# Performance work log

Hardware: AMD Instinct MI355X
Metric: run time of the kernel (lower is better)

The kernel has to match this reference:

```python
import jax, jax.numpy as jnp
import numpy as np

BS, C, H, W = 2, 128, 80, 160
P, G = 9, 8
GC = C // G
EPS = 1e-5


def _layernorm_c(x, g, b):
    # x: (bs, C, H, W); LayerNorm over channel dim (to_3d dim=2 -> norm over c)
    m = jnp.mean(x, axis=1, keepdims=True)
    v = jnp.mean((x - m) ** 2, axis=1, keepdims=True)
    return (x - m) / jnp.sqrt(v + EPS) * g[None, :, None, None] + b[None, :, None, None]


def _conv1x1(x, w, b):
    return jnp.einsum('bchw,oc->bohw', x, w) + b[None, :, None, None]


def _bilinear_sample(feat, pts):
    # feat (bs,C,H,W); pts (bs,N,2) normalized [0,1]; zero padding outside (DAF convention)
    bs, c, h, w = feat.shape
    x = pts[..., 0] * w - 0.5
    y = pts[..., 1] * h - 0.5
    x0 = jnp.floor(x)
    y0 = jnp.floor(y)
    dx = x - x0
    dy = y - y0
    x0i = x0.astype(jnp.int32)
    y0i = y0.astype(jnp.int32)

    def corner(xi, yi, wgt):
        valid = (xi >= 0) & (xi < w) & (yi >= 0) & (yi < h)
        xc = jnp.clip(xi, 0, w - 1)
        yc = jnp.clip(yi, 0, h - 1)
        g = jax.vmap(lambda f, yy, xx: f[:, yy, xx].T)(feat, yc, xc)  # (bs,N,C)
        return g * (wgt * valid)[..., None]

    return (corner(x0i, y0i, (1 - dx) * (1 - dy))
            + corner(x0i + 1, y0i, dx * (1 - dy))
            + corner(x0i, y0i + 1, (1 - dx) * dy)
            + corner(x0i + 1, y0i + 1, dx * dy))


def _branch(match_flat, anchor, feat_value, wmap, kp_w, kp_b):
    bs = feat_value.shape[0]
    hw = H * W
    # Sparse1DKeyPointsGenerator: learned 1D offsets along the disparity (x) direction
    off = match_flat @ kp_w.T + kp_b  # (bs, HW, P)
    anc = anchor.reshape(bs, hw, P, 2)
    kp = jnp.stack([anc[..., 0] + off, anc[..., 1]], axis=-1)  # (bs,HW,P,2)
    # group-softmax attention weights over num_pts
    wts = wmap.transpose(0, 2, 3, 1).reshape(bs, hw, P, G)  # channel c = p*G + g
    wts = jax.nn.softmax(wts, axis=2)
    # deformable aggregation: bilinear gather at key points + group-weighted sum over pts
    sampled = _bilinear_sample(feat_value, kp.reshape(bs, hw * P, 2))
    sampled = sampled.reshape(bs, hw, P, G, GC)
    out = jnp.einsum('bnpgc,bnpg->bngc', sampled, wts).reshape(bs, hw, C)
    out = out.reshape(bs, H, W, C).transpose(0, 3, 1, 2)
    return out, kp


def _forward(mask, match, context, geometric, context_anchor_points, geometric_anchor_points,
             ln_g, ln_b, lnc_g, lnc_b, lng_g, lng_b,
             wc_w, wc_b, wg_w, wg_b, vc_w, vc_b, vg_w, vg_b,
             out_w, out_b, kpc_w, kpc_b, kpg_w, kpg_b):
    bs = match.shape[0]
    hw = H * W
    match_n = _layernorm_c(match, ln_g, ln_b)
    context_n = _layernorm_c(context, lnc_g, lnc_b)
    geometric_n = _layernorm_c(geometric, lng_g, lng_b)
    ctx_val = _conv1x1(context_n, vc_w, vc_b)
    geo_val = _conv1x1(geometric_n, vg_w, vg_b)
    match_flat = match_n.reshape(bs, C, hw).transpose(0, 2, 1)  # (bs,HW,C)
    wc = _conv1x1(match_n, wc_w, wc_b)  # (bs,G*P,H,W)
    wg = _conv1x1(match_n, wg_w, wg_b)
    ctx_out, ctx_kp = _branch(match_flat, context_anchor_points, ctx_val, wc, kpc_w, kpc_b)
    geo_out, geo_kp = _branch(match_flat, geometric_anchor_points, geo_val, wg, kpg_w, kpg_b)
    out = jnp.concatenate([ctx_out * mask, geo_out], axis=1)
    out = _conv1x1(out, out_w, out_b)  # proj_drop is identity (p=0)
    return out, ctx_kp.reshape(bs, H, W, P, 2), geo_kp.reshape(bs, H, W, P, 2)


def setup_inputs() -> dict:
    key = jax.random.key(0)
    ks = jax.random.split(key, 20)

    def wn(k, shape):
        return jax.random.normal(k, shape, jnp.float32) * 0.02

    return {
        'mask': jax.random.uniform(ks[0], (BS, 1, H, W), jnp.float32),
        'match': jax.random.normal(ks[1], (BS, C, H, W), jnp.float32),
        'context': jax.random.normal(ks[2], (BS, C, H, W), jnp.float32),
        'geometric': jax.random.normal(ks[3], (BS, C, H, W), jnp.float32),
        'context_anchor_points': jax.random.uniform(ks[4], (BS, H, W, P, 2), jnp.float32),
        'geometric_anchor_points': jax.random.uniform(ks[5], (BS, H, W, P, 2), jnp.float32),
        'ln_g': jnp.ones((C,), jnp.float32), 'ln_b': jnp.zeros((C,), jnp.float32),
        'lnc_g': jnp.ones((C,), jnp.float32), 'lnc_b': jnp.zeros((C,), jnp.float32),
        'lng_g': jnp.ones((C,), jnp.float32), 'lng_b': jnp.zeros((C,), jnp.float32),
        'wc_w': wn(ks[6], (G * P, C)), 'wc_b': jnp.zeros((G * P,), jnp.float32),
        'wg_w': wn(ks[7], (G * P, C)), 'wg_b': jnp.zeros((G * P,), jnp.float32),
        'vc_w': wn(ks[8], (C, C)), 'vc_b': jnp.zeros((C,), jnp.float32),
        'vg_w': wn(ks[9], (C, C)), 'vg_b': jnp.zeros((C,), jnp.float32),
        'out_w': wn(ks[10], (C, 2 * C)), 'out_b': jnp.zeros((C,), jnp.float32),
        'kpc_w': wn(ks[11], (P, C)), 'kpc_b': jnp.zeros((P,), jnp.float32),
        'kpg_w': wn(ks[12], (P, C)), 'kpg_b': jnp.zeros((P,), jnp.float32),
    }


def reference(mask, match, context, geometric, context_anchor_points, geometric_anchor_points,
              ln_g, ln_b, lnc_g, lnc_b, lng_g, lng_b,
              wc_w, wc_b, wg_w, wg_b, vc_w, vc_b, vg_w, vg_b,
              out_w, out_b, kpc_w, kpc_b, kpg_w, kpg_b):
    return _forward(mask, match, context, geometric, context_anchor_points, geometric_anchor_points,
                    ln_g, ln_b, lnc_g, lnc_b, lng_g, lng_b,
                    wc_w, wc_b, wg_w, wg_b, vc_w, vc_b, vg_w, vg_b,
                    out_w, out_b, kpc_w, kpc_b, kpg_w, kpg_b)
```

## Files before the change

kernel.cpp:

```cpp
#include <hip/hip_runtime.h>
#include <hip/hip_bf16.h>

typedef __hip_bfloat16 bf16;
typedef __bf16 b16x8 __attribute__((ext_vector_type(8)));
typedef float f32x4 __attribute__((ext_vector_type(4)));

#define HWs   12800
#define NPIX  25600
#define IMG_H 80
#define IMG_W 160

#define OFF_VCB  0
#define OFF_VGB  16384
#define OFF_MATB 32768
#define OFF_OUTB 53504
#define NW_BF16  86272

__global__ __launch_bounds__(256) void k_prep(
    const float* __restrict__ vc_w, const float* __restrict__ vg_w,
    const float* __restrict__ wc_w, const float* __restrict__ wg_w,
    const float* __restrict__ kpc_w, const float* __restrict__ kpg_w,
    const float* __restrict__ out_w,
    const float* __restrict__ wc_b, const float* __restrict__ wg_b,
    const float* __restrict__ kpc_b, const float* __restrict__ kpg_b,
    bf16* __restrict__ wbuf, float* __restrict__ bias176)
{
    int i = blockIdx.x * 256 + threadIdx.x;
    if (i < 16384) {
        wbuf[i] = __float2bfloat16(vc_w[i]);
    } else if (i < 32768) {
        wbuf[i] = __float2bfloat16(vg_w[i - 16384]);
    } else if (i < 53504) {
        int j = i - 32768; int row = j >> 7; int c = j & 127;
        float v;
        if (row < 72)       v = wc_w[row * 128 + c];
        else if (row < 144) v = wg_w[(row - 72) * 128 + c];
        else if (row < 153) v = kpc_w[(row - 144) * 128 + c];
        else                v = kpg_w[(row - 153) * 128 + c];
        wbuf[i] = __float2bfloat16(v);
    } else if (i < NW_BF16) {
        wbuf[i] = __float2bfloat16(out_w[i - 53504]);
    } else if (i < NW_BF16 + 176) {
        int j = i - NW_BF16;
        float v = 0.f;
        if (j < 72)       v = wc_b[j];
        else if (j < 144) v = wg_b[j - 72];
        else if (j < 153) v = kpc_b[j - 144];
        else if (j < 162) v = kpg_b[j - 153];
        bias176[j] = v;
    }
}

__global__ __launch_bounds__(256) void k_stage1(
    const float* __restrict__ match, const float* __restrict__ context, const float* __restrict__ geometric,
    const float* __restrict__ ln_g, const float* __restrict__ ln_b,
    const float* __restrict__ lnc_g, const float* __restrict__ lnc_b,
    const float* __restrict__ lng_g, const float* __restrict__ lng_b,
    const float* __restrict__ vc_b, const float* __restrict__ vg_b,
    const bf16* __restrict__ wbuf, const float* __restrict__ bias176,
    const float* __restrict__ anc_c, const float* __restrict__ anc_g,
    bf16* __restrict__ ctx_val, bf16* __restrict__ geo_val,
    bf16* __restrict__ wts_g, float* __restrict__ coords_g,
    float* __restrict__ kp_out)
{
    __shared__ __align__(16) bf16 tile_s[32 * 136];
    __shared__ bf16 logit_s[32 * 144];
    __shared__ float offs_s[32 * 18];
    __shared__ float red1[8][32];
    __shared__ float red2[8][32];

    int bx = blockIdx.x;
    int seg = bx / 800;
    int tile = bx - seg * 800;
    int t = threadIdx.x;
    int pixbase = tile * 32;

    const float* X  = (seg == 0) ? context : (seg == 1) ? geometric : match;
    const float* gg = (seg == 0) ? lnc_g   : (seg == 1) ? lng_g     : ln_g;
    const float* bb = (seg == 0) ? lnc_b   : (seg == 1) ? lng_b     : ln_b;

    int p = t & 31;
    int cq = t >> 5;
    int b = pixbase >= HWs;
    int hw = pixbase - b * HWs;
    const float* base = X + ((size_t)b * 128) * HWs + hw + p;
    float xv[16];
#pragma unroll
    for (int j = 0; j < 16; j++) xv[j] = base[(size_t)(cq * 16 + j) * HWs];

    int wv = t >> 6;
    int lane = t & 63;
    int s = wv >> 1;
    int h = wv & 1;
    int lrow = lane & 15;
    int lq = lane >> 4;
    const bf16* Wb = (seg == 0) ? wbuf + OFF_VCB
                   : (seg == 1) ? wbuf + OFF_VGB
                                : wbuf + OFF_MATB;
    b16x8 wf[4][4];
    float bpre[4];
#pragma unroll
    for (int i = 0; i < 4; i++) {
        int o = (h + 2 * i) * 16 + lrow;
        const bf16* wr = Wb + (size_t)o * 128;
#pragma unroll
        for (int kk = 0; kk < 4; kk++)
            wf[i][kk] = *(const b16x8*)(wr + (kk * 4 + lq) * 8);
        bpre[i] = (seg == 0) ? vc_b[o] : (seg == 1) ? vg_b[o] : bias176[o];
    }

    {
        float s1 = 0.f, s2 = 0.f;
#pragma unroll
        for (int j = 0; j < 16; j++) { s1 += xv[j]; s2 += xv[j] * xv[j]; }
        red1[cq][p] = s1; red2[cq][p] = s2;
        __syncthreads();
        float S1 = 0.f, S2 = 0.f;
#pragma unroll
        for (int q = 0; q < 8; q++) { S1 += red1[q][p]; S2 += red2[q][p]; }
        float mean = S1 * (1.f / 128.f);
        float var  = fmaxf(S2 * (1.f / 128.f) - mean * mean, 0.f);
        float rstd = rsqrtf(var + 1e-5f);
#pragma unroll
        for (int j = 0; j < 16; j++) {
            int c = cq * 16 + j;
            float y = (xv[j] - mean) * rstd * gg[c] + bb[c];
            tile_s[p * 136 + c] = __float2bfloat16(y);
        }
        __syncthreads();
    }

    const b16x8* arow = (const b16x8*)(tile_s + (s * 16 + lrow) * 136);
    b16x8 af[4];
#pragma unroll
    for (int kk = 0; kk < 4; kk++) af[kk] = arow[kk * 4 + lq];

    if (seg < 2) {
        bf16* val = (seg == 0) ? ctx_val : geo_val;
#pragma unroll
        for (int i = 0; i < 4; i++) {
            int o = (h + 2 * i) * 16 + lrow;
            f32x4 acc = {0.f, 0.f, 0.f, 0.f};
#pragma unroll
            for (int kk = 0; kk < 4; kk++)
                acc = __builtin_amdgcn_mfma_f32_16x16x32_bf16(af[kk], wf[i][kk], acc, 0, 0, 0);
#pragma unroll
            for (int r = 0; r < 4; r++) {
                int pix = pixbase + s * 16 + lq * 4 + r;
                val[(size_t)pix * 128 + o] = __float2bfloat16(acc[r] + bpre[i]);
            }
        }
        return;
    }

#pragma unroll
    for (int i = 0; i < 4; i++) {
        int o = (h + 2 * i) * 16 + lrow;
        f32x4 acc = {0.f, 0.f, 0.f, 0.f};
#pragma unroll
        for (int kk = 0; kk < 4; kk++)
            acc = __builtin_amdgcn_mfma_f32_16x16x32_bf16(af[kk], wf[i][kk], acc, 0, 0, 0);
#pragma unroll
        for (int r = 0; r < 4; r++) {
            int row = s * 16 + lq * 4 + r;
            logit_s[row * 144 + o] = __float2bfloat16(acc[r] + bpre[i]);
        }
    }
    for (int ot = h + 8; ot < 11; ot += 2) {
        int o = ot * 16 + lrow;
        const bf16* wr = Wb + (size_t)o * 128;
        f32x4 acc = {0.f, 0.f, 0.f, 0.f};
#pragma unroll
        for (int kk = 0; kk < 4; kk++)
            acc = __builtin_amdgcn_mfma_f32_16x16x32_bf16(af[kk], *(const b16x8*)(wr + (kk * 4 + lq) * 8), acc, 0, 0, 0);
        float bias = bias176[o];
#pragma unroll
        for (int r = 0; r < 4; r++) {
            int row = s * 16 + lq * 4 + r;
            float v = acc[r] + bias;
            if (o < 144)       logit_s[row * 144 + o] = __float2bfloat16(v);
            else if (o < 162)  offs_s[row * 18 + (o - 144)] = v;
        }
    }
    __syncthreads();

#pragma unroll
    for (int i = 0; i < 2; i++) {
        int task = t + 256 * i;
        int lp = task >> 4;
        int sub = task & 15;
        int br = sub >> 3;
        int g = sub & 7;
        const bf16* basel = logit_s + lp * 144 + br * 72 + g;
        float v[9];
        float m = -1e30f;
#pragma unroll
        for (int pp = 0; pp < 9; pp++) { v[pp] = __bfloat162float(basel[pp * 8]); m = fmaxf(m, v[pp]); }
        float ssum = 0.f;
#pragma unroll
        for (int pp = 0; pp < 9; pp++) { v[pp] = __expf(v[pp] - m); ssum += v[pp]; }
        float inv = 1.f / ssum;
        int pix = pixbase + lp;
        bf16* wbp = wts_g + ((size_t)pix * 2 + br) * 72 + g * 9;
#pragma unroll
        for (int pp = 0; pp < 9; pp++) wbp[pp] = __float2bfloat16(v[pp] * inv);
    }

    for (int i = 0; i < 3; i++) {
        int task = t + 256 * i;
        if (task < 576) {
            int lp = task / 18;
            int sub = task - lp * 18;
            int br = sub / 9;
            int pp = sub - br * 9;
            int pix = pixbase + lp;
            float off = offs_s[lp * 18 + br * 9 + pp];
            const float* anc = br ? anc_g : anc_c;
            float ax = anc[(size_t)pix * 18 + pp * 2];
            float ay = anc[(size_t)pix * 18 + pp * 2 + 1];
            float kx = ax + off;
            float* kpo = kp_out + (size_t)br * (NPIX * 18) + (size_t)pix * 18 + pp * 2;
            kpo[0] = kx;
            kpo[1] = ay;
            float* cbp = coords_g + ((size_t)pix * 2 + br) * 18 + pp * 2;
            cbp[0] = kx * 160.f - 0.5f;
            cbp[1] = ay * 80.f - 0.5f;
        }
    }
}

__global__ __launch_bounds__(256) void k_aggout(
    const bf16* __restrict__ ctx_val, const bf16* __restrict__ geo_val,
    const bf16* __restrict__ wts_g, const float* __restrict__ coords_g,
    const float* __restrict__ mask,
    const bf16* __restrict__ outb, const float* __restrict__ out_b,
    float* __restrict__ out)
{
    __shared__ __align__(16) bf16 smem[32 * 264];
    int t = threadIdx.x;
    int wv = t >> 6;
    int lane = t & 63;
    int q = lane >> 4;
    int sub = lane & 15;
    int c0 = sub * 8;
    int g = sub >> 1;
    int pixbase = blockIdx.x * 32;
    int b = pixbase >= HWs;
    int rowbase = b * HWs;
    int qwid = wv * 4 + q;

    for (int i = 0; i < 4; i++) {
        int task = i * 16 + qwid;
        int lp = task >> 1;
        int br = task & 1;
        int pix = pixbase + lp;
        int tk = pix * 2 + br;
        const bf16* val = br ? geo_val : ctx_val;
        const float* cb = coords_g + (size_t)tk * 18;
        const bf16* wb = wts_g + (size_t)tk * 72 + g * 9;
        float wtv[9];
#pragma unroll
        for (int pp = 0; pp < 9; pp++) wtv[pp] = __bfloat162float(wb[pp]);
        float acc[8] = {0.f, 0.f, 0.f, 0.f, 0.f, 0.f, 0.f, 0.f};
        for (int pp = 0; pp < 9; pp++) {
            float px = cb[pp * 2];
            float py = cb[pp * 2 + 1];
            float fx = floorf(px), fy = floorf(py);
            float dx = px - fx, dy = py - fy;
            int x0 = (int)fx, y0 = (int)fy;
            float wt = wtv[pp];
#pragma unroll
            for (int c4 = 0; c4 < 4; c4++) {
                int xi = x0 + (c4 & 1);
                int yi = y0 + (c4 >> 1);
                bool ok = (xi >= 0) & (xi < IMG_W) & (yi >= 0) & (yi < IMG_H);
                int xc = min(max(xi, 0), IMG_W - 1);
                int yc = min(max(yi, 0), IMG_H - 1);
                float wx = (c4 & 1) ? dx : 1.f - dx;
                float wy = (c4 >> 1) ? dy : 1.f - dy;
                float wgt = ok ? wx * wy * wt : 0.f;
                b16x8 v = *(const b16x8*)(val + (size_t)(rowbase + yc * IMG_W + xc) * 128 + c0);
#pragma unroll
                for (int j = 0; j < 8; j++) acc[j] += wgt * (float)v[j];
            }
        }
        float mv = (br == 0) ? mask[pix] : 1.f;
        b16x8 pk;
#pragma unroll
        for (int j = 0; j < 8; j++) pk[j] = (__bf16)(acc[j] * mv);
        *(b16x8*)(smem + lp * 264 + br * 128 + c0) = pk;
    }
    __syncthreads();

    int s = wv >> 1;
    int h = wv & 1;
    int lrow = lane & 15;
    int lq = lane >> 4;
    const b16x8* arow = (const b16x8*)(smem + (s * 16 + lrow) * 264);
    b16x8 af[8];
#pragma unroll
    for (int kk = 0; kk < 8; kk++) af[kk] = arow[kk * 4 + lq];
#pragma unroll
    for (int i = 0; i < 4; i++) {
        int o = (h + 2 * i) * 16 + lrow;
        const bf16* wrow = outb + (size_t)o * 256;
        f32x4 acc = {0.f, 0.f, 0.f, 0.f};
#pragma unroll
        for (int kk = 0; kk < 8; kk++)
            acc = __builtin_amdgcn_mfma_f32_16x16x32_bf16(af[kk], *(const b16x8*)(wrow + (kk * 4 + lq) * 8), acc, 0, 0, 0);
        float bias = out_b[o];
#pragma unroll
        for (int r = 0; r < 4; r++) {
            int pix = pixbase + s * 16 + lq * 4 + r;
            int hw = pix - b * HWs;
            out[(size_t)b * (128 * HWs) + (size_t)o * HWs + hw] = acc[r] + bias;
        }
    }
}

extern "C" void kernel_launch(void* const* d_in, const int* in_sizes, int n_in,
                              void* d_out, int out_size, void* d_ws, size_t ws_size,
                              hipStream_t stream)
{
    const float* mask      = (const float*)d_in[0];
    const float* match     = (const float*)d_in[1];
    const float* context   = (const float*)d_in[2];
    const float* geometric = (const float*)d_in[3];
    const float* anc_c     = (const float*)d_in[4];
    const float* anc_g     = (const float*)d_in[5];
    const float* ln_g  = (const float*)d_in[6];
    const float* ln_b  = (const float*)d_in[7];
    const float* lnc_g = (const float*)d_in[8];
    const float* lnc_b = (const float*)d_in[9];
    const float* lng_g = (const float*)d_in[10];
    const float* lng_b = (const float*)d_in[11];
    const float* wc_w  = (const float*)d_in[12];
    const float* wc_b  = (const float*)d_in[13];
    const float* wg_w  = (const float*)d_in[14];
    const float* wg_b  = (const float*)d_in[15];
    const float* vc_w  = (const float*)d_in[16];
    const float* vc_b  = (const float*)d_in[17];
    const float* vg_w  = (const float*)d_in[18];
    const float* vg_b  = (const float*)d_in[19];
    const float* out_w = (const float*)d_in[20];
    const float* out_b = (const float*)d_in[21];
    const float* kpc_w = (const float*)d_in[22];
    const float* kpc_b = (const float*)d_in[23];
    const float* kpg_w = (const float*)d_in[24];
    const float* kpg_b = (const float*)d_in[25];

    char* w = (char*)d_ws;
    bf16*  ctx_val  = (bf16*)(w);
    bf16*  geo_val  = (bf16*)(w + 6553600);
    bf16*  wts_g    = (bf16*)(w + 13107200);
    float* coords_g = (float*)(w + 20480000);
    bf16*  wbuf     = (bf16*)(w + 24166400);
    float* bias176  = (float*)(w + 24338944);

    float* outp = (float*)d_out;
    float* kp_out = outp + (size_t)2 * 128 * HWs;

    k_prep<<<(NW_BF16 + 176 + 255) / 256, 256, 0, stream>>>(
        vc_w, vg_w, wc_w, wg_w, kpc_w, kpg_w, out_w,
        wc_b, wg_b, kpc_b, kpg_b, wbuf, bias176);
    k_stage1<<<2400, 256, 0, stream>>>(match, context, geometric,
                                       ln_g, ln_b, lnc_g, lnc_b, lng_g, lng_b,
                                       vc_b, vg_b, wbuf, bias176,
                                       anc_c, anc_g,
                                       ctx_val, geo_val, wts_g, coords_g, kp_out);
    k_aggout<<<800, 256, 0, stream>>>(ctx_val, geo_val, wts_g, coords_g, mask,
                                      wbuf + OFF_OUTB, out_b, outp);
}
```

Baseline: 222.2 us.

## Store value maps in fp8 and split aggregation from output projection

```diff
diff --git a/kernel.cpp b/kernel.cpp
--- a/kernel.cpp
+++ b/kernel.cpp
@@ -4,6 +4,7 @@
 typedef __hip_bfloat16 bf16;
 typedef __bf16 b16x8 __attribute__((ext_vector_type(8)));
 typedef float f32x4 __attribute__((ext_vector_type(4)));
+typedef float f32x2 __attribute__((ext_vector_type(2)));
 
 #define HWs   12800
 #define NPIX  25600
@@ -15,6 +16,11 @@
 #define OFF_MATB 32768
 #define OFF_OUTB 53504
 #define NW_BF16  86272
+
+static __device__ inline unsigned char enc_fp8(float v)
+{
+    return (unsigned char)(__builtin_amdgcn_cvt_pk_fp8_f32(v, v, 0, false) & 0xFF);
+}
 
 __global__ __launch_bounds__(256) void k_prep(
     const float* __restrict__ vc_w, const float* __restrict__ vg_w,
@@ -59,7 +65,7 @@
     const float* __restrict__ vc_b, const float* __restrict__ vg_b,
     const bf16* __restrict__ wbuf, const float* __restrict__ bias176,
     const float* __restrict__ anc_c, const float* __restrict__ anc_g,
-    bf16* __restrict__ ctx_val, bf16* __restrict__ geo_val,
+    unsigned char* __restrict__ ctx8, unsigned char* __restrict__ geo8,
     bf16* __restrict__ wts_g, float* __restrict__ coords_g,
     float* __restrict__ kp_out)
 {
@@ -136,7 +142,7 @@
     for (int kk = 0; kk < 4; kk++) af[kk] = arow[kk * 4 + lq];
 
     if (seg < 2) {
-        bf16* val = (seg == 0) ? ctx_val : geo_val;
+        unsigned char* val = (seg == 0) ? ctx8 : geo8;
 #pragma unroll
         for (int i = 0; i < 4; i++) {
             int o = (h + 2 * i) * 16 + lrow;
@@ -147,7 +153,7 @@
 #pragma unroll
             for (int r = 0; r < 4; r++) {
                 int pix = pixbase + s * 16 + lq * 4 + r;
-                val[(size_t)pix * 128 + o] = __float2bfloat16(acc[r] + bpre[i]);
+                val[(size_t)pix * 128 + o] = enc_fp8(acc[r] + bpre[i]);
             }
         }
         return;
@@ -229,14 +235,12 @@
     }
 }
 
-__global__ __launch_bounds__(256) void k_aggout(
-    const bf16* __restrict__ ctx_val, const bf16* __restrict__ geo_val,
+__global__ __launch_bounds__(256) void k_agg(
+    const unsigned char* __restrict__ ctx8, const unsigned char* __restrict__ geo8,
     const bf16* __restrict__ wts_g, const float* __restrict__ coords_g,
     const float* __restrict__ mask,
-    const bf16* __restrict__ outb, const float* __restrict__ out_b,
-    float* __restrict__ out)
-{
-    __shared__ __align__(16) bf16 smem[32 * 264];
+    bf16* __restrict__ aggf)
+{
     int t = threadIdx.x;
     int wv = t >> 6;
     int lane = t & 63;
@@ -244,62 +248,78 @@
     int sub = lane & 15;
     int c0 = sub * 8;
     int g = sub >> 1;
+
+    int bx = blockIdx.x;
+    int xcd = bx & 7;
+    int br = xcd >> 2;
+    int grp = (bx >> 3) * 4 + (xcd & 3);
+    int pix = grp * 16 + wv * 4 + q;
+    int tk = pix * 2 + br;
+    int b = pix >= HWs;
+    int rowbase = b * HWs;
+
+    const unsigned char* val = br ? geo8 : ctx8;
+    const float* cb = coords_g + (size_t)tk * 18;
+    const bf16* wb = wts_g + (size_t)tk * 72 + g * 9;
+
+    float wtv[9];
+#pragma unroll
+    for (int pp = 0; pp < 9; pp++) wtv[pp] = __bfloat162float(wb[pp]);
+
+    float acc[8] = {0.f, 0.f, 0.f, 0.f, 0.f, 0.f, 0.f, 0.f};
+    for (int pp = 0; pp < 9; pp++) {
+        float px = cb[pp * 2];
+        float py = cb[pp * 2 + 1];
+        float fx = floorf(px), fy = floorf(py);
+        float dx = px - fx, dy = py - fy;
+        int x0 = (int)fx, y0 = (int)fy;
+        float wt = wtv[pp];
+#pragma unroll
+        for (int c4 = 0; c4 < 4; c4++) {
+            int xi = x0 + (c4 & 1);
+            int yi = y0 + (c4 >> 1);
+            bool ok = (xi >= 0) & (xi < IMG_W) & (yi >= 0) & (yi < IMG_H);
+            int xc = min(max(xi, 0), IMG_W - 1);
+            int yc = min(max(yi, 0), IMG_H - 1);
+            float wx = (c4 & 1) ? dx : 1.f - dx;
+            float wy = (c4 >> 1) ? dy : 1.f - dy;
+            float wgt = ok ? wx * wy * wt : 0.f;
+            uint2 u = *(const uint2*)(val + (size_t)(rowbase + yc * IMG_W + xc) * 128 + c0);
+            f32x2 v01 = __builtin_amdgcn_cvt_pk_f32_fp8(u.x, false);
+            f32x2 v23 = __builtin_amdgcn_cvt_pk_f32_fp8(u.x, true);
+            f32x2 v45 = __builtin_amdgcn_cvt_pk_f32_fp8(u.y, false);
+            f32x2 v67 = __builtin_amdgcn_cvt_pk_f32_fp8(u.y, true);
+            acc[0] += wgt * v01[0]; acc[1] += wgt * v01[1];
+            acc[2] += wgt * v23[0]; acc[3] += wgt * v23[1];
+            acc[4] += wgt * v45[0]; acc[5] += wgt * v45[1];
+            acc[6] += wgt * v67[0]; acc[7] += wgt * v67[1];
+        }
+    }
+    float mv = (br == 0) ? mask[pix] : 1.f;
+    b16x8 pk;
+#pragma unroll
+    for (int j = 0; j < 8; j++) pk[j] = (__bf16)(acc[j] * mv);
+    *(b16x8*)(aggf + (size_t)pix * 256 + br * 128 + c0) = pk;
+}
+
+__global__ __launch_bounds__(256) void k_out(
+    const bf16* __restrict__ aggf,
+    const bf16* __restrict__ outb, const float* __restrict__ out_b,
+    float* __restrict__ out)
+{
+    int t = threadIdx.x;
     int pixbase = blockIdx.x * 32;
-    int b = pixbase >= HWs;
-    int rowbase = b * HWs;
-    int qwid = wv * 4 + q;
-
-    for (int i = 0; i < 4; i++) {
-        int task = i * 16 + qwid;
-        int lp = task >> 1;
-        int br = task & 1;
-        int pix = pixbase + lp;
-        int tk = pix * 2 + br;
-        const bf16* val = br ? geo_val : ctx_val;
-        const float* cb = coords_g + (size_t)tk * 18;
-        const bf16* wb = wts_g + (size_t)tk * 72 + g * 9;
-        float wtv[9];
-#pragma unroll
-        for (int pp = 0; pp < 9; pp++) wtv[pp] = __bfloat162float(wb[pp]);
-        float acc[8] = {0.f, 0.f, 0.f, 0.f, 0.f, 0.f, 0.f, 0.f};
-        for (int pp = 0; pp < 9; pp++) {
-            float px = cb[pp * 2];
-            float py = cb[pp * 2 + 1];
-            float fx = floorf(px), fy = floorf(py);
-            float dx = px - fx, dy = py - fy;
-            int x0 = (int)fx, y0 = (int)fy;
-            float wt = wtv[pp];
-#pragma unroll
-            for (int c4 = 0; c4 < 4; c4++) {
-                int xi = x0 + (c4 & 1);
-                int yi = y0 + (c4 >> 1);
-                bool ok = (xi >= 0) & (xi < IMG_W) & (yi >= 0) & (yi < IMG_H);
-                int xc = min(max(xi, 0), IMG_W - 1);
-                int yc = min(max(yi, 0), IMG_H - 1);
-                float wx = (c4 & 1) ? dx : 1.f - dx;
-                float wy = (c4 >> 1) ? dy : 1.f - dy;
-                float wgt = ok ? wx * wy * wt : 0.f;
-                b16x8 v = *(const b16x8*)(val + (size_t)(rowbase + yc * IMG_W + xc) * 128 + c0);
-#pragma unroll
-                for (int j = 0; j < 8; j++) acc[j] += wgt * (float)v[j];
-            }
-        }
-        float mv = (br == 0) ? mask[pix] : 1.f;
-        b16x8 pk;
-#pragma unroll
-        for (int j = 0; j < 8; j++) pk[j] = (__bf16)(acc[j] * mv);
-        *(b16x8*)(smem + lp * 264 + br * 128 + c0) = pk;
-    }
-    __syncthreads();
-
+    int wv = t >> 6;
+    int lane = t & 63;
     int s = wv >> 1;
     int h = wv & 1;
     int lrow = lane & 15;
     int lq = lane >> 4;
-    const b16x8* arow = (const b16x8*)(smem + (s * 16 + lrow) * 264);
+    const b16x8* arow = (const b16x8*)(aggf + (size_t)(pixbase + s * 16 + lrow) * 256);
     b16x8 af[8];
 #pragma unroll
     for (int kk = 0; kk < 8; kk++) af[kk] = arow[kk * 4 + lq];
+    int b = pixbase >= HWs;
 #pragma unroll
     for (int i = 0; i < 4; i++) {
         int o = (h + 2 * i) * 16 + lrow;
@@ -350,12 +370,13 @@
     const float* kpg_b = (const float*)d_in[25];
 
     char* w = (char*)d_ws;
-    bf16*  ctx_val  = (bf16*)(w);
-    bf16*  geo_val  = (bf16*)(w + 6553600);
-    bf16*  wts_g    = (bf16*)(w + 13107200);
-    float* coords_g = (float*)(w + 20480000);
-    bf16*  wbuf     = (bf16*)(w + 24166400);
-    float* bias176  = (float*)(w + 24338944);
+    unsigned char* ctx8 = (unsigned char*)(w);
+    unsigned char* geo8 = (unsigned char*)(w + 3276800);
+    bf16*  wts_g    = (bf16*)(w + 6553600);
+    float* coords_g = (float*)(w + 13926400);
+    bf16*  aggf     = (bf16*)(w + 17612800);
+    bf16*  wbuf     = (bf16*)(w + 30720000);
+    float* bias176  = (float*)(w + 30892544);
 
     float* outp = (float*)d_out;
     float* kp_out = outp + (size_t)2 * 128 * HWs;
@@ -367,7 +388,7 @@
                                        ln_g, ln_b, lnc_g, lnc_b, lng_g, lng_b,
                                        vc_b, vg_b, wbuf, bias176,
                                        anc_c, anc_g,
-                                       ctx_val, geo_val, wts_g, coords_g, kp_out);
-    k_aggout<<<800, 256, 0, stream>>>(ctx_val, geo_val, wts_g, coords_g, mask,
-                                      wbuf + OFF_OUTB, out_b, outp);
-}
+                                       ctx8, geo8, wts_g, coords_g, kp_out);
+    k_agg<<<3200, 256, 0, stream>>>(ctx8, geo8, wts_g, coords_g, mask, aggf);
+    k_out<<<800, 256, 0, stream>>>(aggf, wbuf + OFF_OUTB, out_b, outp);
+}
```

New measurement: 203.6 us. 1.09x faster.
